# Kernel tuning notes

Measured on AMD Instinct MI355X. Metric: run time of the kernel, lower is better.

## Reference

```python
import jax, jax.numpy as jnp
import numpy as np

B, SQ, SKV, D = 4, 4096, 4096, 64

def setup_inputs() -> dict:
    key = jax.random.key(0)
    kq, kk, kv = jax.random.split(key, 3)
    return {
        "q": jax.random.normal(kq, (B, SQ, D), dtype=jnp.float32),
        "k": jax.random.normal(kk, (B, SKV, D), dtype=jnp.float32),
        "v": jax.random.normal(kv, (B, SKV, D), dtype=jnp.float32),
        "inv_scale_factor": 8,
        "is_training": 0,
    }

def reference(q, k, v, inv_scale_factor, is_training):
    # qk = q @ k^T, divided by inv_scale_factor, softmax over keys
    scores = jnp.einsum("bqd,bkd->bqk", q, k) / inv_scale_factor  # [B,SQ,SKV]
    attn = jax.nn.softmax(scores, axis=-1)
    # dropout is deterministic identity (eval mode, is_training=0)
    out = jnp.einsum("bqk,bkd->bqd", attn, v)  # [B,SQ,D]
    # should_apply_residual before loop
    out = out + q
    # 3-iteration chain: residual add + normalization add (+2q), dropout (identity),
    # sigmoid, clamp(0,1)
    for _ in range(3):
        out = out + 2.0 * q
        out = jax.nn.sigmoid(out)
        out = jnp.clip(out, 0.0, 1.0)
    return out
```

## Files before the change

kernel.cpp:

```cpp
#include <hip/hip_runtime.h>

#define SQd 4096
#define SKVd 4096
#define DDIM 64
#define BK 32
#define NG 8
#define NTILES (SKVd / BK)
#define TPG (NTILES / NG)
#define TILE_BYTES 2048
#define KWS_BYTES (4 * NTILES * TILE_BYTES)
#define BROWS 32

typedef float floatx4 __attribute__((ext_vector_type(4)));

__device__ inline long long mk64(int lo, int hi) {
    int2 t; t.x = lo; t.y = hi;
    return __builtin_bit_cast(long long, t);
}
template <bool HI>
__device__ inline int pk2(float a, float b, int old) {
    return __builtin_amdgcn_cvt_pk_fp8_f32(a, b, old, HI);
}

struct CombS {
    float Ored[BROWS][4][68];
    float Lred[BROWS][NG];
};

__global__ __launch_bounds__(256)
void prepack_kernel(const float* __restrict__ k, const float* __restrict__ v,
                    char* __restrict__ ws)
{
    __shared__ __align__(16) float Kt[BK][68];
    __shared__ __align__(16) float Vt[BK][68];

    const int blk  = blockIdx.x;
    const int b    = blk >> 7;
    const int tile = blk & (NTILES - 1);
    const int tid  = threadIdx.x;

    const size_t base = ((size_t)b * SKVd + tile * BK) * DDIM;
    {
        const int row = tid >> 3, col = (tid & 7) * 8;
        const float4 k0 = *(const float4*)(k + base + (size_t)row * DDIM + col);
        const float4 k1 = *(const float4*)(k + base + (size_t)row * DDIM + col + 4);
        *(float4*)&Kt[row][col] = k0; *(float4*)&Kt[row][col + 4] = k1;
        const float4 v0 = *(const float4*)(v + base + (size_t)row * DDIM + col);
        const float4 v1 = *(const float4*)(v + base + (size_t)row * DDIM + col + 4);
        *(float4*)&Vt[row][col] = v0; *(float4*)&Vt[row][col + 4] = v1;
    }
    __syncthreads();

    const int lane = tid & 63;
    const int l16  = lane & 15;
    const int quad = lane >> 4;
    const int f    = tid >> 6;

    int w[4];
    size_t off;
    if (f < 2) {
        const float* s0 = &Kt[f * 16 + l16][quad * 8];
        const float* s1 = &Kt[f * 16 + l16][32 + quad * 8];
        w[0] = pk2<false>(s0[0], s0[1], 0); w[0] = pk2<true>(s0[2], s0[3], w[0]);
        w[1] = pk2<false>(s0[4], s0[5], 0); w[1] = pk2<true>(s0[6], s0[7], w[1]);
        w[2] = pk2<false>(s1[0], s1[1], 0); w[2] = pk2<true>(s1[2], s1[3], w[2]);
        w[3] = pk2<false>(s1[4], s1[5], 0); w[3] = pk2<true>(s1[6], s1[7], w[3]);
        off = ((size_t)(b * NTILES + tile) * 2 + f) * 1024 + lane * 16;
    } else {
        const int p = f - 2;
        float vv[16];
        #pragma unroll
        for (int j2 = 0; j2 < 16; ++j2) {
            const int nb = 2 * p + (j2 >> 3);
            const int j  = j2 & 7;
            vv[j2] = Vt[16 * (j >> 2) + quad * 4 + (j & 3)][nb * 16 + l16];
        }
        #pragma unroll
        for (int i = 0; i < 4; ++i) {
            w[i] = pk2<false>(vv[4 * i], vv[4 * i + 1], 0);
            w[i] = pk2<true>(vv[4 * i + 2], vv[4 * i + 3], w[i]);
        }
        off = (size_t)KWS_BYTES + ((size_t)(b * NTILES + tile) * 2 + p) * 1024 + lane * 16;
    }
    int4 o4; o4.x = w[0]; o4.y = w[1]; o4.z = w[2]; o4.w = w[3];
    *(int4*)(ws + off) = o4;
}

__global__ __launch_bounds__(512, 4)
void fattn_kernel(const float* __restrict__ q, const int* __restrict__ isf_p,
                  const char* __restrict__ kws, const char* __restrict__ vws,
                  float* __restrict__ out)
{
    __shared__ __align__(16) CombS C;

    const int tid  = threadIdx.x;
    const int g    = tid >> 6;
    const int lane = tid & 63;
    const int l16  = lane & 15;
    const int quad = lane >> 4;

    const int bidx  = blockIdx.x;
    const int b     = bidx >> 7;
    const int qbase = (bidx & 127) * BROWS;

    const float scale = 1.44269504088896340736f / (float)(*isf_p);
    const float SINIT = -4.0f * 1.44269504088896340736f;

    long long qf[2][2];
    #pragma unroll
    for (int qg = 0; qg < 2; ++qg) {
        const int qrow = qbase + qg * 16 + l16;
        const float* qp = q + ((size_t)b * SQd + qrow) * DDIM + quad * 8;
        #pragma unroll
        for (int dh = 0; dh < 2; ++dh) {
            const float4 a0 = *(const float4*)(qp + dh * 32);
            const float4 a1 = *(const float4*)(qp + dh * 32 + 4);
            int lo = pk2<false>(a0.x * scale, a0.y * scale, 0);
            lo     = pk2<true>(a0.z * scale, a0.w * scale, lo);
            int hi = pk2<false>(a1.x * scale, a1.y * scale, 0);
            hi     = pk2<true>(a1.z * scale, a1.w * scale, hi);
            qf[qg][dh] = mk64(lo, hi);
        }
    }

    const char* kg = kws + (size_t)(b * NTILES + g * TPG) * TILE_BYTES + lane * 16;
    const char* vg = vws + (size_t)(b * NTILES + g * TPG) * TILE_BYTES + lane * 16;
    const int phase = bidx & (TPG - 1);

    floatx4 o[2][4];
    float l_acc[2];
    #pragma unroll
    for (int qg = 0; qg < 2; ++qg) {
        l_acc[qg] = 0.0f;
        #pragma unroll
        for (int nb = 0; nb < 4; ++nb)
            #pragma unroll
            for (int r = 0; r < 4; ++r) o[qg][nb][r] = 0.0f;
    }
    const floatx4 sinit = {SINIT, SINIT, SINIT, SINIT};

    auto load = [&](int4* kd, int4* vd, int t) {
        const size_t off = (size_t)((t + phase) & (TPG - 1)) * TILE_BYTES;
        kd[0] = *(const int4*)(kg + off);
        kd[1] = *(const int4*)(kg + off + 1024);
        vd[0] = *(const int4*)(vg + off);
        vd[1] = *(const int4*)(vg + off + 1024);
    };
    auto compute = [&](const int4* kc, const int4* vc) {
        const long long k00 = mk64(kc[0].x, kc[0].y), k01 = mk64(kc[0].z, kc[0].w);
        const long long k10 = mk64(kc[1].x, kc[1].y), k11 = mk64(kc[1].z, kc[1].w);
        const long long v0 = mk64(vc[0].x, vc[0].y), v1 = mk64(vc[0].z, vc[0].w);
        const long long v2 = mk64(vc[1].x, vc[1].y), v3 = mk64(vc[1].z, vc[1].w);
        #pragma unroll
        for (int qg = 0; qg < 2; ++qg) {
            floatx4 s0 = sinit, s1 = sinit;
            s0 = __builtin_amdgcn_mfma_f32_16x16x32_fp8_fp8(k00, qf[qg][0], s0, 0, 0, 0);
            s0 = __builtin_amdgcn_mfma_f32_16x16x32_fp8_fp8(k01, qf[qg][1], s0, 0, 0, 0);
            s1 = __builtin_amdgcn_mfma_f32_16x16x32_fp8_fp8(k10, qf[qg][0], s1, 0, 0, 0);
            s1 = __builtin_amdgcn_mfma_f32_16x16x32_fp8_fp8(k11, qf[qg][1], s1, 0, 0, 0);
            const float p00 = __builtin_amdgcn_exp2f(s0[0]);
            const float p01 = __builtin_amdgcn_exp2f(s0[1]);
            const float p02 = __builtin_amdgcn_exp2f(s0[2]);
            const float p03 = __builtin_amdgcn_exp2f(s0[3]);
            const float p10 = __builtin_amdgcn_exp2f(s1[0]);
            const float p11 = __builtin_amdgcn_exp2f(s1[1]);
            const float p12 = __builtin_amdgcn_exp2f(s1[2]);
            const float p13 = __builtin_amdgcn_exp2f(s1[3]);
            l_acc[qg] += (p00 + p01) + (p02 + p03) + (p10 + p11) + (p12 + p13);
            int lo = pk2<false>(p00, p01, 0); lo = pk2<true>(p02, p03, lo);
            int hi = pk2<false>(p10, p11, 0); hi = pk2<true>(p12, p13, hi);
            const long long pf = mk64(lo, hi);
            o[qg][0] = __builtin_amdgcn_mfma_f32_16x16x32_fp8_fp8(pf, v0, o[qg][0], 0, 0, 0);
            o[qg][1] = __builtin_amdgcn_mfma_f32_16x16x32_fp8_fp8(pf, v1, o[qg][1], 0, 0, 0);
            o[qg][2] = __builtin_amdgcn_mfma_f32_16x16x32_fp8_fp8(pf, v2, o[qg][2], 0, 0, 0);
            o[qg][3] = __builtin_amdgcn_mfma_f32_16x16x32_fp8_fp8(pf, v3, o[qg][3], 0, 0, 0);
        }
    };

    int4 kb0[2], vb0[2], kb1[2], vb1[2];
    load(kb0, vb0, 0);
    #pragma unroll
    for (int t = 0; t < TPG / 2; ++t) {
        load(kb1, vb1, 2 * t + 1);
        compute(kb0, vb0);
        load(kb0, vb0, (2 * t + 2) & (TPG - 1));
        compute(kb1, vb1);
    }

    #pragma unroll
    for (int qg = 0; qg < 2; ++qg) {
        l_acc[qg] += __shfl_xor(l_acc[qg], 16);
        l_acc[qg] += __shfl_xor(l_acc[qg], 32);
    }
    if (quad == 0) {
        #pragma unroll
        for (int qg = 0; qg < 2; ++qg)
            C.Lred[qg * 16 + l16][g] = l_acc[qg];
    }

    if (g < 4) {
        #pragma unroll
        for (int qg = 0; qg < 2; ++qg)
            #pragma unroll
            for (int nb = 0; nb < 4; ++nb)
                #pragma unroll
                for (int r = 0; r < 4; ++r)
                    C.Ored[qg * 16 + quad * 4 + r][g][nb * 16 + l16] = o[qg][nb][r];
    }
    __syncthreads();
    if (g >= 4) {
        #pragma unroll
        for (int qg = 0; qg < 2; ++qg)
            #pragma unroll
            for (int nb = 0; nb < 4; ++nb)
                #pragma unroll
                for (int r = 0; r < 4; ++r)
                    C.Ored[qg * 16 + quad * 4 + r][g - 4][nb * 16 + l16] += o[qg][nb][r];
    }
    __syncthreads();

    {
        const int row = tid >> 4;
        const int d4  = (tid & 15) * 4;
        float l = 0.0f;
        #pragma unroll
        for (int gg = 0; gg < NG; ++gg) l += C.Lred[row][gg];
        const float rl = 1.0f / l;
        float xs[4] = {0.f, 0.f, 0.f, 0.f};
        #pragma unroll
        for (int s = 0; s < 4; ++s) {
            const float4 t4 = *(const float4*)&C.Ored[row][s][d4];
            xs[0] += t4.x; xs[1] += t4.y; xs[2] += t4.z; xs[3] += t4.w;
        }
        const size_t idx = ((size_t)b * SQd + qbase + row) * DDIM + d4;
        const float4 q4 = *(const float4*)(q + idx);
        const float qs[4] = {q4.x, q4.y, q4.z, q4.w};
        #pragma unroll
        for (int c = 0; c < 4; ++c) {
            float x = xs[c] * rl + qs[c];
            #pragma unroll
            for (int itc = 0; itc < 3; ++itc) {
                x = x + 2.0f * qs[c];
                x = 1.0f / (1.0f + __expf(-x));
                x = fminf(fmaxf(x, 0.0f), 1.0f);
            }
            xs[c] = x;
        }
        const float4 r4 = {xs[0], xs[1], xs[2], xs[3]};
        *(float4*)(out + idx) = r4;
    }
}

extern "C" void kernel_launch(void* const* d_in, const int* in_sizes, int n_in,
                              void* d_out, int out_size, void* d_ws, size_t ws_size,
                              hipStream_t stream) {
    const float* q = (const float*)d_in[0];
    const float* k = (const float*)d_in[1];
    const float* v = (const float*)d_in[2];
    const int* isf = (const int*)d_in[3];
    float* out = (float*)d_out;
    char* ws = (char*)d_ws;

    prepack_kernel<<<dim3(4 * NTILES), dim3(256), 0, stream>>>(k, v, ws);

    const int nblocks = 4 * (SQd / BROWS);
    fattn_kernel<<<dim3(nblocks), dim3(512), 0, stream>>>(
        q, isf, ws, ws + KWS_BYTES, out);
}
```

Baseline: 87.44 us.

## Process K/V tiles in pairs with split K and V prefetch

Replaces the per-tile double-buffered loop with a macro step that handles two tiles at once. The K loads for the next pair are issued before the QK/exp phase and the V loads before the PV phase, so each load has more work to hide behind and the QK MFMAs of both tiles are grouped. It also drops the per-block phase rotation of the tile order, so all blocks now walk tiles in the same sequence, and it adds register pressure from the larger buffers. Note TPG is 16 (8 pairs), while the loop does 8 macro steps, the last one reloading pair 7 redundantly.

```diff
diff --git a/kernel.cpp b/kernel.cpp
--- a/kernel.cpp
+++ b/kernel.cpp
@@ -125,7 +125,6 @@
 
     const char* kg = kws + (size_t)(b * NTILES + g * TPG) * TILE_BYTES + lane * 16;
     const char* vg = vws + (size_t)(b * NTILES + g * TPG) * TILE_BYTES + lane * 16;
-    const int phase = bidx & (TPG - 1);
 
     floatx4 o[2][4];
     float l_acc[2];
@@ -139,52 +138,69 @@
     }
     const floatx4 sinit = {SINIT, SINIT, SINIT, SINIT};
 
-    auto load = [&](int4* kd, int4* vd, int t) {
-        const size_t off = (size_t)((t + phase) & (TPG - 1)) * TILE_BYTES;
-        kd[0] = *(const int4*)(kg + off);
-        kd[1] = *(const int4*)(kg + off + 1024);
-        vd[0] = *(const int4*)(vg + off);
-        vd[1] = *(const int4*)(vg + off + 1024);
+    auto loadPair = [&](int4* d, const char* base_p, int pair) {
+        const size_t off = (size_t)pair * (2 * TILE_BYTES);
+        d[0] = *(const int4*)(base_p + off);
+        d[1] = *(const int4*)(base_p + off + 1024);
+        d[2] = *(const int4*)(base_p + off + 2048);
+        d[3] = *(const int4*)(base_p + off + 3072);
     };
-    auto compute = [&](const int4* kc, const int4* vc) {
-        const long long k00 = mk64(kc[0].x, kc[0].y), k01 = mk64(kc[0].z, kc[0].w);
-        const long long k10 = mk64(kc[1].x, kc[1].y), k11 = mk64(kc[1].z, kc[1].w);
-        const long long v0 = mk64(vc[0].x, vc[0].y), v1 = mk64(vc[0].z, vc[0].w);
-        const long long v2 = mk64(vc[1].x, vc[1].y), v3 = mk64(vc[1].z, vc[1].w);
-        #pragma unroll
-        for (int qg = 0; qg < 2; ++qg) {
-            floatx4 s0 = sinit, s1 = sinit;
-            s0 = __builtin_amdgcn_mfma_f32_16x16x32_fp8_fp8(k00, qf[qg][0], s0, 0, 0, 0);
-            s0 = __builtin_amdgcn_mfma_f32_16x16x32_fp8_fp8(k01, qf[qg][1], s0, 0, 0, 0);
-            s1 = __builtin_amdgcn_mfma_f32_16x16x32_fp8_fp8(k10, qf[qg][0], s1, 0, 0, 0);
-            s1 = __builtin_amdgcn_mfma_f32_16x16x32_fp8_fp8(k11, qf[qg][1], s1, 0, 0, 0);
-            const float p00 = __builtin_amdgcn_exp2f(s0[0]);
-            const float p01 = __builtin_amdgcn_exp2f(s0[1]);
-            const float p02 = __builtin_amdgcn_exp2f(s0[2]);
-            const float p03 = __builtin_amdgcn_exp2f(s0[3]);
-            const float p10 = __builtin_amdgcn_exp2f(s1[0]);
-            const float p11 = __builtin_amdgcn_exp2f(s1[1]);
-            const float p12 = __builtin_amdgcn_exp2f(s1[2]);
-            const float p13 = __builtin_amdgcn_exp2f(s1[3]);
-            l_acc[qg] += (p00 + p01) + (p02 + p03) + (p10 + p11) + (p12 + p13);
-            int lo = pk2<false>(p00, p01, 0); lo = pk2<true>(p02, p03, lo);
-            int hi = pk2<false>(p10, p11, 0); hi = pk2<true>(p12, p13, hi);
-            const long long pf = mk64(lo, hi);
-            o[qg][0] = __builtin_amdgcn_mfma_f32_16x16x32_fp8_fp8(pf, v0, o[qg][0], 0, 0, 0);
-            o[qg][1] = __builtin_amdgcn_mfma_f32_16x16x32_fp8_fp8(pf, v1, o[qg][1], 0, 0, 0);
-            o[qg][2] = __builtin_amdgcn_mfma_f32_16x16x32_fp8_fp8(pf, v2, o[qg][2], 0, 0, 0);
-            o[qg][3] = __builtin_amdgcn_mfma_f32_16x16x32_fp8_fp8(pf, v3, o[qg][3], 0, 0, 0);
+
+    auto macro = [&](const int4* ck, const int4* cv, int4* nk, int4* nv, int pn) {
+        loadPair(nk, kg, pn);
+        long long pf[2][2];
+        #pragma unroll
+        for (int i = 0; i < 2; ++i) {
+            const long long k00 = mk64(ck[2*i].x,   ck[2*i].y);
+            const long long k01 = mk64(ck[2*i].z,   ck[2*i].w);
+            const long long k10 = mk64(ck[2*i+1].x, ck[2*i+1].y);
+            const long long k11 = mk64(ck[2*i+1].z, ck[2*i+1].w);
+            #pragma unroll
+            for (int qg = 0; qg < 2; ++qg) {
+                floatx4 s0 = sinit, s1 = sinit;
+                s0 = __builtin_amdgcn_mfma_f32_16x16x32_fp8_fp8(k00, qf[qg][0], s0, 0, 0, 0);
+                s0 = __builtin_amdgcn_mfma_f32_16x16x32_fp8_fp8(k01, qf[qg][1], s0, 0, 0, 0);
+                s1 = __builtin_amdgcn_mfma_f32_16x16x32_fp8_fp8(k10, qf[qg][0], s1, 0, 0, 0);
+                s1 = __builtin_amdgcn_mfma_f32_16x16x32_fp8_fp8(k11, qf[qg][1], s1, 0, 0, 0);
+                const float p00 = __builtin_amdgcn_exp2f(s0[0]);
+                const float p01 = __builtin_amdgcn_exp2f(s0[1]);
+                const float p02 = __builtin_amdgcn_exp2f(s0[2]);
+                const float p03 = __builtin_amdgcn_exp2f(s0[3]);
+                const float p10 = __builtin_amdgcn_exp2f(s1[0]);
+                const float p11 = __builtin_amdgcn_exp2f(s1[1]);
+                const float p12 = __builtin_amdgcn_exp2f(s1[2]);
+                const float p13 = __builtin_amdgcn_exp2f(s1[3]);
+                l_acc[qg] += (p00 + p01) + (p02 + p03) + (p10 + p11) + (p12 + p13);
+                int lo = pk2<false>(p00, p01, 0); lo = pk2<true>(p02, p03, lo);
+                int hi = pk2<false>(p10, p11, 0); hi = pk2<true>(p12, p13, hi);
+                pf[i][qg] = mk64(lo, hi);
+            }
+        }
+        loadPair(nv, vg, pn);
+        #pragma unroll
+        for (int i = 0; i < 2; ++i) {
+            const long long v0 = mk64(cv[2*i].x,   cv[2*i].y);
+            const long long v1 = mk64(cv[2*i].z,   cv[2*i].w);
+            const long long v2 = mk64(cv[2*i+1].x, cv[2*i+1].y);
+            const long long v3 = mk64(cv[2*i+1].z, cv[2*i+1].w);
+            #pragma unroll
+            for (int qg = 0; qg < 2; ++qg) {
+                o[qg][0] = __builtin_amdgcn_mfma_f32_16x16x32_fp8_fp8(pf[i][qg], v0, o[qg][0], 0, 0, 0);
+                o[qg][1] = __builtin_amdgcn_mfma_f32_16x16x32_fp8_fp8(pf[i][qg], v1, o[qg][1], 0, 0, 0);
+                o[qg][2] = __builtin_amdgcn_mfma_f32_16x16x32_fp8_fp8(pf[i][qg], v2, o[qg][2], 0, 0, 0);
+                o[qg][3] = __builtin_amdgcn_mfma_f32_16x16x32_fp8_fp8(pf[i][qg], v3, o[qg][3], 0, 0, 0);
+            }
         }
     };
 
-    int4 kb0[2], vb0[2], kb1[2], vb1[2];
-    load(kb0, vb0, 0);
-    #pragma unroll
-    for (int t = 0; t < TPG / 2; ++t) {
-        load(kb1, vb1, 2 * t + 1);
-        compute(kb0, vb0);
-        load(kb0, vb0, (2 * t + 2) & (TPG - 1));
-        compute(kb1, vb1);
+    int4 kA[4], vA[4], kB[4], vB[4];
+    loadPair(kA, kg, 0);
+    loadPair(vA, vg, 0);
+    #pragma unroll
+    for (int mm = 0; mm < 4; ++mm) {
+        macro(kA, vA, kB, vB, 2 * mm + 1);
+        const int nxt = (2 * mm + 2 < 8) ? 2 * mm + 2 : 7;
+        macro(kB, vB, kA, vA, nxt);
     }
 
     #pragma unroll
```

Measured after the change: 88.66 us. About the same (+1.4%).

## Use triple-buffered K/V register prefetch and drop per-block tile phase rotation

Applied to the files above, without the earlier changes.

Replaces the double-buffered load/compute loop with a three-slot register ring that prefetches two tiles ahead, so global load latency has more time to hide behind MFMA work. It also removes the per-block phase offset that rotated the tile start order, so all blocks now walk tiles in the same order. The old loop also issued one redundant wrap-around load at the end, which is gone. This costs more VGPRs for the extra buffer, which could reduce occupancy, and losing the staggering may concentrate memory traffic on the same addresses.

```diff
diff --git a/kernel.cpp b/kernel.cpp
--- a/kernel.cpp
+++ b/kernel.cpp
@@ -125,7 +125,6 @@
 
     const char* kg = kws + (size_t)(b * NTILES + g * TPG) * TILE_BYTES + lane * 16;
     const char* vg = vws + (size_t)(b * NTILES + g * TPG) * TILE_BYTES + lane * 16;
-    const int phase = bidx & (TPG - 1);
 
     floatx4 o[2][4];
     float l_acc[2];
@@ -139,14 +138,18 @@
     }
     const floatx4 sinit = {SINIT, SINIT, SINIT, SINIT};
 
-    auto load = [&](int4* kd, int4* vd, int t) {
-        const size_t off = (size_t)((t + phase) & (TPG - 1)) * TILE_BYTES;
-        kd[0] = *(const int4*)(kg + off);
-        kd[1] = *(const int4*)(kg + off + 1024);
-        vd[0] = *(const int4*)(vg + off);
-        vd[1] = *(const int4*)(vg + off + 1024);
+    int4 kb[3][2], vb[3][2];
+
+    auto loadTile = [&](int slot, int t) {
+        const size_t off = (size_t)t * TILE_BYTES;
+        kb[slot][0] = *(const int4*)(kg + off);
+        kb[slot][1] = *(const int4*)(kg + off + 1024);
+        vb[slot][0] = *(const int4*)(vg + off);
+        vb[slot][1] = *(const int4*)(vg + off + 1024);
     };
-    auto compute = [&](const int4* kc, const int4* vc) {
+    auto compute = [&](int slot) {
+        const int4* kc = kb[slot];
+        const int4* vc = vb[slot];
         const long long k00 = mk64(kc[0].x, kc[0].y), k01 = mk64(kc[0].z, kc[0].w);
         const long long k10 = mk64(kc[1].x, kc[1].y), k11 = mk64(kc[1].z, kc[1].w);
         const long long v0 = mk64(vc[0].x, vc[0].y), v1 = mk64(vc[0].z, vc[0].w);
@@ -177,14 +180,12 @@
         }
     };
 
-    int4 kb0[2], vb0[2], kb1[2], vb1[2];
-    load(kb0, vb0, 0);
-    #pragma unroll
-    for (int t = 0; t < TPG / 2; ++t) {
-        load(kb1, vb1, 2 * t + 1);
-        compute(kb0, vb0);
-        load(kb0, vb0, (2 * t + 2) & (TPG - 1));
-        compute(kb1, vb1);
+    loadTile(0, 0);
+    loadTile(1, 1);
+    #pragma unroll
+    for (int t = 0; t < TPG; ++t) {
+        if (t + 2 < TPG) loadTile((t + 2) % 3, t + 2);
+        compute(t % 3);
     }
 
     #pragma unroll
```

After: 89.65 us. +2.5%, slower.
